# Kernel optimization log

Measured on AMD Instinct MI355X. Metric: run time of the kernel, lower is better.

Reference implementation:

```python
import jax, jax.numpy as jnp
import numpy as np

V = 256  # vec_size
B = 128  # batch
T = 1024  # seq_len


def _lstm_layer(x_seq, W_ih, W_hh, b_ih, b_hh):
    # x_seq: [B, T, V]; weights follow torch LSTMCell layout: W_* [4V, V], gate order i,f,g,o
    x_proj = jnp.einsum('btv,gv->btg', x_seq, W_ih) + b_ih + b_hh  # [B, T, 4V]
    x_proj = jnp.transpose(x_proj, (1, 0, 2))  # time-major [T, B, 4V]
    Bsz = x_seq.shape[0]
    Vd = W_hh.shape[1]
    h0 = jnp.zeros((Bsz, Vd), x_seq.dtype)
    c0 = jnp.zeros((Bsz, Vd), x_seq.dtype)

    def step(carry, xp):
        h, c = carry
        gates = xp + h @ W_hh.T  # [B, 4V]
        i, f, g, o = jnp.split(gates, 4, axis=-1)
        i = jax.nn.sigmoid(i)
        f = jax.nn.sigmoid(f)
        g = jnp.tanh(g)
        o = jax.nn.sigmoid(o)
        c = f * c + i * g
        h = o * jnp.tanh(c)
        return (h, c), h

    _, hs = jax.lax.scan(step, (h0, c0), x_proj)  # hs: [T, B, V]
    return jnp.transpose(hs, (1, 0, 2))  # [B, T, V]


def setup_inputs() -> dict:
    key = jax.random.key(0)
    ks = jax.random.split(key, 12)
    s = 1.0 / np.sqrt(V)  # torch LSTMCell / Linear init scale
    u = lambda k, shape: jax.random.uniform(k, shape, jnp.float32, -s, s)
    return {
        'x': jax.random.normal(ks[0], (B, T, V), jnp.float32),
        'W_ih1': u(ks[1], (4 * V, V)), 'W_hh1': u(ks[2], (4 * V, V)),
        'b_ih1': u(ks[3], (4 * V,)), 'b_hh1': u(ks[4], (4 * V,)),
        'W_ih2': u(ks[5], (4 * V, V)), 'W_hh2': u(ks[6], (4 * V, V)),
        'b_ih2': u(ks[7], (4 * V,)), 'b_hh2': u(ks[8], (4 * V,)),
        'fc_w': u(ks[9], (V, V)), 'fc_b': u(ks[10], (V,)),
    }


def reference(x, W_ih1, W_hh1, b_ih1, b_hh1, W_ih2, W_hh2, b_ih2, b_hh2, fc_w, fc_b):
    h1s = _lstm_layer(x, W_ih1, W_hh1, b_ih1, b_hh1)      # [B, T, V]
    h2s = _lstm_layer(h1s, W_ih2, W_hh2, b_ih2, b_hh2)    # [B, T, V]
    # NormalizedLinear: linear with L2 row-normalized weight
    w_n = fc_w / jnp.linalg.norm(fc_w, axis=1, keepdims=True)
    out = jnp.einsum('btv,ov->bto', h2s, w_n) + fc_b
    return out
```

## Files before the change

kernel.cpp:

```cpp
#include <hip/hip_runtime.h>
#include <stdint.h>

#define Tt 1024
#define Bt 128
#define Vt 256
#define TS 32768

typedef __attribute__((ext_vector_type(8))) short bf16x8;
typedef __attribute__((ext_vector_type(4))) float f32x4;
typedef __attribute__((ext_vector_type(4))) int i32x4;

#define MFMA(a, b, c) __builtin_amdgcn_mfma_f32_16x16x32_bf16(a, b, c, 0, 0, 0)
#define SENT 0x7FFF


__device__ __forceinline__ unsigned short f2bf(float f) {
    unsigned u = __builtin_bit_cast(unsigned, f);
    u += 0x7fffu + ((u >> 16) & 1u);
    return (unsigned short)(u >> 16);
}
__device__ __forceinline__ float sigm(float x) {
    return __builtin_amdgcn_rcpf(1.f + __expf(-x));
}
__device__ __forceinline__ float tanh_f(float x) {
    float e = __expf(-2.f * fabsf(x));
    float t = (1.f - e) * __builtin_amdgcn_rcpf(1.f + e);
    return copysignf(t, x);
}

template <int OFF>
__device__ __forceinline__ bf16x8 ldcc(const unsigned short* p) {
    bf16x8 d;
    asm volatile("global_load_dwordx4 %0, %1, off offset:%c2 sc0 sc1"
                 : "=v"(d) : "v"(p), "i"(OFF));
    return d;
}
#define LD8T(d, P)                                        \
    do {                                                  \
        const unsigned short* _p2 = (P) + 2048;           \
        d[0] = ldcc<0>(P);      d[1] = ldcc<1024>(P);     \
        d[2] = ldcc<2048>(P);   d[3] = ldcc<3072>(P);     \
        d[4] = ldcc<0>(_p2);    d[5] = ldcc<1024>(_p2);   \
        d[6] = ldcc<2048>(_p2); d[7] = ldcc<3072>(_p2);   \
    } while (0)

__device__ __forceinline__ void vm_drain() {
    asm volatile("s_waitcnt vmcnt(0)" ::: "memory");
    __builtin_amdgcn_sched_barrier(0);
}
__device__ __forceinline__ int fdirty(bf16x8 f) {
    i32x4 d = __builtin_bit_cast(i32x4, f);
    return ((d.x & 0xFFFF) == SENT) | ((d.z & 0xFFFF) == SENT);
}

__global__ __launch_bounds__(256) void cvt_kernel(const float* __restrict__ x,
                                                  unsigned short* __restrict__ xT) {
    unsigned g = blockIdx.x * 256u + threadIdx.x;
    unsigned base = g * 8u;
    unsigned r = base >> 8;
    unsigned v = base & 255u;
    unsigned t = r >> 7, b = r & 127u;
    const float4* src = (const float4*)(x + ((size_t)b * Tt + t) * Vt + v);
    float4 f0 = src[0], f1 = src[1];
    union { unsigned short s[8]; int4 q; } o;
    o.s[0] = f2bf(f0.x); o.s[1] = f2bf(f0.y); o.s[2] = f2bf(f0.z); o.s[3] = f2bf(f0.w);
    o.s[4] = f2bf(f1.x); o.s[5] = f2bf(f1.y); o.s[6] = f2bf(f1.z); o.s[7] = f2bf(f1.w);
    *(int4*)(xT + (size_t)r * Vt + v) = o.q;
}

__global__ __launch_bounds__(256) void fill_kernel(unsigned short* __restrict__ h) {
    size_t i = ((size_t)blockIdx.x * 256u + threadIdx.x) * 16u;
    i32x4 s = (i32x4){0x7FFF7FFF, 0x7FFF7FFF, 0x7FFF7FFF, 0x7FFF7FFF};
    *(i32x4*)(h + i) = s;
    *(i32x4*)(h + i + 8) = s;
}

__global__ __launch_bounds__(256) void rec_kernel(
    const float* __restrict__ Wih1, const float* __restrict__ Whh1,
    const float* __restrict__ bih1, const float* __restrict__ bhh1,
    const float* __restrict__ Wih2, const float* __restrict__ Whh2,
    const float* __restrict__ bih2, const float* __restrict__ bhh2,
    const unsigned short* __restrict__ xT,
    unsigned short* h1s, unsigned short* h2s) {
    const int bid = blockIdx.x;
    const int layer = bid >> 6;
    const int cgrp = (bid >> 3) & 7;
    const int bgrp = bid & 7;

    const float* Win = layer ? Wih2 : Wih1;
    const float* Whh = layer ? Whh2 : Whh1;
    const float* bi = layer ? bih2 : bih1;
    const float* bh = layer ? bhh2 : bhh1;

    __shared__ unsigned short sW[2][128][264];
    __shared__ float sG[4][16][36];
    __shared__ unsigned short sH[16][32];

    const int tid = threadIdx.x;
    {
        int row = tid >> 1, seg = (tid & 1) * 128;
        size_t grow = (size_t)(256 * (row >> 5) + 32 * cgrp + (row & 31)) * Vt + seg;
        for (int m = 0; m < 2; ++m) {
            const float* src = (m ? Whh : Win) + grow;
            unsigned short* dst = &sW[m][row][seg];
            for (int k = 0; k < 128; k += 4) {
                float4 f = *(const float4*)(src + k);
                dst[k + 0] = f2bf(f.x); dst[k + 1] = f2bf(f.y);
                dst[k + 2] = f2bf(f.z); dst[k + 3] = f2bf(f.w);
            }
        }
    }
    __syncthreads();

    const int lane = tid & 63;
    const int wv = tid >> 6;
    const int q = lane >> 4;
    const int ln = lane & 15;

    float biasv[2];
#pragma unroll
    for (int n = 0; n < 2; ++n) {
        int grow = 256 * wv + 32 * cgrp + n * 16 + ln;
        biasv[n] = bi[grow] + bh[grow];
    }
    const int cb = tid >> 4;
    const int cc0 = (tid & 15) * 2;
    float cst[2] = {0.f, 0.f};

    const int aoff = ln * 32 + q * 8;
    const size_t hbase = (size_t)bgrp * 4096 + aoff;
    const int xoff = (16 * bgrp + ln) * 256 + q * 8;
    unsigned short* ob = layer ? h2s : h1s;
    unsigned short* sptr = ob + (size_t)bgrp * 4096 + cgrp * 512 + lane * 8;

    for (int t = 0; t < Tt; ++t) {
        f32x4 acc[2];
        acc[0] = (f32x4){biasv[0], biasv[0], biasv[0], biasv[0]};
        acc[1] = (f32x4){biasv[1], biasv[1], biasv[1], biasv[1]};
        bf16x8 a1[8], a2[8];

        if (layer == 0) {
            const unsigned short* xp = xT + (size_t)t * TS + xoff;
#pragma unroll
            for (int kb = 0; kb < 8; ++kb) a1[kb] = *(const bf16x8*)(xp + kb * 32);
            const unsigned short* hp = h1s + (size_t)(t - 1) * TS + hbase;
            if (t > 0) LD8T(a2, hp);
#pragma unroll
            for (int kb = 0; kb < 8; ++kb) {
                bf16x8 b0 = *(const bf16x8*)&sW[0][32 * wv + ln][kb * 32 + q * 8];
                bf16x8 b1 = *(const bf16x8*)&sW[0][32 * wv + 16 + ln][kb * 32 + q * 8];
                acc[0] = MFMA(a1[kb], b0, acc[0]);
                acc[1] = MFMA(a1[kb], b1, acc[1]);
            }
            if (t > 0) {
                for (;;) {
                    vm_drain();
                    int d = 0;
#pragma unroll
                    for (int kb = 0; kb < 8; ++kb) d |= fdirty(a2[kb]);
                    if (!__any(d)) break;
                    __builtin_amdgcn_s_sleep(1);
                    LD8T(a2, hp);
                }
#pragma unroll
                for (int kb = 0; kb < 8; ++kb) {
                    bf16x8 b0 = *(const bf16x8*)&sW[1][32 * wv + ln][kb * 32 + q * 8];
                    bf16x8 b1 = *(const bf16x8*)&sW[1][32 * wv + 16 + ln][kb * 32 + q * 8];
                    acc[0] = MFMA(a2[kb], b0, acc[0]);
                    acc[1] = MFMA(a2[kb], b1, acc[1]);
                }
            }
        } else {
            const unsigned short* hp1 = h1s + (size_t)t * TS + hbase;
            const unsigned short* hp2 = h2s + (size_t)(t - 1) * TS + hbase;
            LD8T(a1, hp1);
            if (t > 0) LD8T(a2, hp2);
            unsigned need = (t > 0) ? 3u : 1u;
            for (;;) {
                vm_drain();
                unsigned nm = 0;
                if (need & 1) {
                    int d = 0;
#pragma unroll
                    for (int kb = 0; kb < 8; ++kb) d |= fdirty(a1[kb]);
                    if (__any(d)) nm |= 1u;
                }
                if (need & 2) {
                    int d = 0;
#pragma unroll
                    for (int kb = 0; kb < 8; ++kb) d |= fdirty(a2[kb]);
                    if (__any(d)) nm |= 2u;
                }
                if (!nm) break;
                need = nm;
                __builtin_amdgcn_s_sleep(1);
                if (nm & 1) LD8T(a1, hp1);
                if (nm & 2) LD8T(a2, hp2);
            }
#pragma unroll
            for (int kb = 0; kb < 8; ++kb) {
                bf16x8 b0 = *(const bf16x8*)&sW[0][32 * wv + ln][kb * 32 + q * 8];
                bf16x8 b1 = *(const bf16x8*)&sW[0][32 * wv + 16 + ln][kb * 32 + q * 8];
                acc[0] = MFMA(a1[kb], b0, acc[0]);
                acc[1] = MFMA(a1[kb], b1, acc[1]);
            }
            if (t > 0) {
#pragma unroll
                for (int kb = 0; kb < 8; ++kb) {
                    bf16x8 b0 = *(const bf16x8*)&sW[1][32 * wv + ln][kb * 32 + q * 8];
                    bf16x8 b1 = *(const bf16x8*)&sW[1][32 * wv + 16 + ln][kb * 32 + q * 8];
                    acc[0] = MFMA(a2[kb], b0, acc[0]);
                    acc[1] = MFMA(a2[kb], b1, acc[1]);
                }
            }
        }

#pragma unroll
        for (int n = 0; n < 2; ++n)
#pragma unroll
            for (int r = 0; r < 4; ++r) sG[wv][q * 4 + r][n * 16 + ln] = acc[n][r];
        __syncthreads();
#pragma unroll
        for (int j = 0; j < 2; ++j) {
            int c = cc0 + j;
            float iv = sG[0][cb][c], fv = sG[1][cb][c];
            float gv = sG[2][cb][c], ov = sG[3][cb][c];
            float cval = sigm(fv) * cst[j] + sigm(iv) * tanh_f(gv);
            cst[j] = cval;
            sH[cb][c] = f2bf(sigm(ov) * tanh_f(cval));
        }
        __syncthreads();
        if (tid < 64) {
            bf16x8 hv = *(const bf16x8*)((const unsigned short*)sH + tid * 8);
            unsigned short* dst = sptr + (size_t)t * TS;
            asm volatile("global_store_dwordx4 %0, %1, off sc0 sc1" ::"v"(dst),
                         "v"(hv) : "memory");
        }
    }
}

__global__ __launch_bounds__(256) void fc_kernel(const unsigned short* __restrict__ h2s,
                                                 const float* __restrict__ fcw,
                                                 const float* __restrict__ fcb,
                                                 float* __restrict__ out) {
    const int bid = blockIdx.x;
    const int rb = bid >> 2;
    const int c0 = (bid & 3) * 64;
    __shared__ unsigned short sWf[64][264];
    __shared__ float sInv[64];
    const int tid = threadIdx.x;
    if (tid < 64) {
        const float* wr = fcw + (size_t)(c0 + tid) * 256;
        float s = 0.f;
        for (int k = 0; k < 256; k += 4) {
            float4 f = *(const float4*)(wr + k);
            s += f.x * f.x + f.y * f.y + f.z * f.z + f.w * f.w;
        }
        sInv[tid] = rsqrtf(s);
    }
    __syncthreads();
    {
        int lr = tid & 63, seg = tid >> 6;
        float inv = sInv[lr];
        const float* wr = fcw + (size_t)(c0 + lr) * 256 + seg * 64;
        unsigned short* dst = &sWf[lr][seg * 64];
        for (int k = 0; k < 64; k += 4) {
            float4 f = *(const float4*)(wr + k);
            dst[k + 0] = f2bf(f.x * inv); dst[k + 1] = f2bf(f.y * inv);
            dst[k + 2] = f2bf(f.z * inv); dst[k + 3] = f2bf(f.w * inv);
        }
    }
    __syncthreads();
    const int lane = tid & 63, w = tid >> 6, q = lane >> 4, ln = lane & 15;
    f32x4 acc[2][4];
    for (int rk = 0; rk < 2; ++rk)
        for (int nb = 0; nb < 4; ++nb) {
            float bv = fcb[c0 + nb * 16 + ln];
            acc[rk][nb] = (f32x4){bv, bv, bv, bv};
        }
    const unsigned short* P0 =
        h2s + (size_t)rb * TS + (2 * w) * 4096 + ln * 32 + q * 8;
    const unsigned short* P1 = P0 + 4096;
    for (int kb = 0; kb < 8; ++kb) {
        bf16x8 a0 = *(const bf16x8*)(P0 + kb * 512);
        bf16x8 a1 = *(const bf16x8*)(P1 + kb * 512);
        for (int nb = 0; nb < 4; ++nb) {
            bf16x8 b = *(const bf16x8*)&sWf[nb * 16 + ln][kb * 32 + q * 8];
            acc[0][nb] = MFMA(a0, b, acc[0][nb]);
            acc[1][nb] = MFMA(a1, b, acc[1][nb]);
        }
    }
    for (int rk = 0; rk < 2; ++rk)
        for (int nb = 0; nb < 4; ++nb)
            for (int r = 0; r < 4; ++r) {
                int bb = 32 * w + rk * 16 + q * 4 + r;
                int o = c0 + nb * 16 + ln;
                out[((size_t)bb * Tt + rb) * 256 + o] = acc[rk][nb][r];
            }
}

extern "C" void kernel_launch(void* const* d_in, const int* in_sizes, int n_in,
                              void* d_out, int out_size, void* d_ws, size_t ws_size,
                              hipStream_t stream) {
    const float* x    = (const float*)d_in[0];
    const float* Wih1 = (const float*)d_in[1];
    const float* Whh1 = (const float*)d_in[2];
    const float* bih1 = (const float*)d_in[3];
    const float* bhh1 = (const float*)d_in[4];
    const float* Wih2 = (const float*)d_in[5];
    const float* Whh2 = (const float*)d_in[6];
    const float* bih2 = (const float*)d_in[7];
    const float* bhh2 = (const float*)d_in[8];
    const float* fcw  = (const float*)d_in[9];
    const float* fcb  = (const float*)d_in[10];

    char* ws = (char*)d_ws;
    unsigned short* xT  = (unsigned short*)ws;
    unsigned short* h1s = xT + (size_t)Tt * TS;
    unsigned short* h2s = h1s + (size_t)Tt * TS;

    fill_kernel<<<16384, 256, 0, stream>>>(h1s);
    cvt_kernel<<<16384, 256, 0, stream>>>(x, xT);
    rec_kernel<<<128, 256, 0, stream>>>(Wih1, Whh1, bih1, bhh1,
                                        Wih2, Whh2, bih2, bhh2,
                                        xT, h1s, h2s);
    fc_kernel<<<4096, 256, 0, stream>>>(h2s, fcw, fcb, (float*)d_out);
}
```

Baseline: 3.107 ms.

## Reorder gate rows per wave so LSTM cell update stays in-wave without block barriers

Weight rows in shared memory are regrouped so each wave holds all four gates (i,f,g,o) for its own 8 hidden columns. The cell update then happens in registers via a lane shuffle instead of through a shared-memory gate exchange. This removes both per-timestep __syncthreads from the recurrent loop, and each wave stores its own h slice. The hidden-state memory layout changes to match, and the FC kernel's addressing is updated to the same layout.

```diff
diff --git a/kernel.cpp b/kernel.cpp
--- a/kernel.cpp
+++ b/kernel.cpp
@@ -92,17 +92,17 @@
     const float* bi = layer ? bih2 : bih1;
     const float* bh = layer ? bhh2 : bhh1;
 
-    __shared__ unsigned short sW[2][128][264];
-    __shared__ float sG[4][16][36];
-    __shared__ unsigned short sH[16][32];
+    __shared__ unsigned short sW[2][4][32][264];
+    __shared__ unsigned short sH[4][16][8];
 
     const int tid = threadIdx.x;
     {
         int row = tid >> 1, seg = (tid & 1) * 128;
-        size_t grow = (size_t)(256 * (row >> 5) + 32 * cgrp + (row & 31)) * Vt + seg;
+        int wvs = row >> 5, lr = row & 31, gate = lr >> 3, loc = lr & 7;
+        size_t grow = (size_t)(256 * gate + 32 * cgrp + 8 * wvs + loc) * Vt + seg;
         for (int m = 0; m < 2; ++m) {
             const float* src = (m ? Whh : Win) + grow;
-            unsigned short* dst = &sW[m][row][seg];
+            unsigned short* dst = &sW[m][wvs][lr][seg];
             for (int k = 0; k < 128; k += 4) {
                 float4 f = *(const float4*)(src + k);
                 dst[k + 0] = f2bf(f.x); dst[k + 1] = f2bf(f.y);
@@ -119,19 +119,18 @@
 
     float biasv[2];
 #pragma unroll
-    for (int n = 0; n < 2; ++n) {
-        int grow = 256 * wv + 32 * cgrp + n * 16 + ln;
-        biasv[n] = bi[grow] + bh[grow];
-    }
-    const int cb = tid >> 4;
-    const int cc0 = (tid & 15) * 2;
-    float cst[2] = {0.f, 0.f};
-
-    const int aoff = ln * 32 + q * 8;
-    const size_t hbase = (size_t)bgrp * 4096 + aoff;
+    for (int nb = 0; nb < 2; ++nb) {
+        int gate = nb * 2 + (ln >> 3);
+        int grow = 256 * gate + 32 * cgrp + 8 * wv + (ln & 7);
+        biasv[nb] = bi[grow] + bh[grow];
+    }
+    float cst[4] = {0.f, 0.f, 0.f, 0.f};
+
+    const size_t hbase = (size_t)bgrp * 4096 + q * 128 + ln * 8;
     const int xoff = (16 * bgrp + ln) * 256 + q * 8;
     unsigned short* ob = layer ? h2s : h1s;
-    unsigned short* sptr = ob + (size_t)bgrp * 4096 + cgrp * 512 + lane * 8;
+    unsigned short* sptr =
+        ob + (size_t)bgrp * 4096 + cgrp * 512 + wv * 128 + lane * 8;
 
     for (int t = 0; t < Tt; ++t) {
         f32x4 acc[2];
@@ -147,8 +146,8 @@
             if (t > 0) LD8T(a2, hp);
 #pragma unroll
             for (int kb = 0; kb < 8; ++kb) {
-                bf16x8 b0 = *(const bf16x8*)&sW[0][32 * wv + ln][kb * 32 + q * 8];
-                bf16x8 b1 = *(const bf16x8*)&sW[0][32 * wv + 16 + ln][kb * 32 + q * 8];
+                bf16x8 b0 = *(const bf16x8*)&sW[0][wv][ln][kb * 32 + q * 8];
+                bf16x8 b1 = *(const bf16x8*)&sW[0][wv][16 + ln][kb * 32 + q * 8];
                 acc[0] = MFMA(a1[kb], b0, acc[0]);
                 acc[1] = MFMA(a1[kb], b1, acc[1]);
             }
@@ -164,8 +163,8 @@
                 }
 #pragma unroll
                 for (int kb = 0; kb < 8; ++kb) {
-                    bf16x8 b0 = *(const bf16x8*)&sW[1][32 * wv + ln][kb * 32 + q * 8];
-                    bf16x8 b1 = *(const bf16x8*)&sW[1][32 * wv + 16 + ln][kb * 32 + q * 8];
+                    bf16x8 b0 = *(const bf16x8*)&sW[1][wv][ln][kb * 32 + q * 8];
+                    bf16x8 b1 = *(const bf16x8*)&sW[1][wv][16 + ln][kb * 32 + q * 8];
                     acc[0] = MFMA(a2[kb], b0, acc[0]);
                     acc[1] = MFMA(a2[kb], b1, acc[1]);
                 }
@@ -199,16 +198,16 @@
             }
 #pragma unroll
             for (int kb = 0; kb < 8; ++kb) {
-                bf16x8 b0 = *(const bf16x8*)&sW[0][32 * wv + ln][kb * 32 + q * 8];
-                bf16x8 b1 = *(const bf16x8*)&sW[0][32 * wv + 16 + ln][kb * 32 + q * 8];
+                bf16x8 b0 = *(const bf16x8*)&sW[0][wv][ln][kb * 32 + q * 8];
+                bf16x8 b1 = *(const bf16x8*)&sW[0][wv][16 + ln][kb * 32 + q * 8];
                 acc[0] = MFMA(a1[kb], b0, acc[0]);
                 acc[1] = MFMA(a1[kb], b1, acc[1]);
             }
             if (t > 0) {
 #pragma unroll
                 for (int kb = 0; kb < 8; ++kb) {
-                    bf16x8 b0 = *(const bf16x8*)&sW[1][32 * wv + ln][kb * 32 + q * 8];
-                    bf16x8 b1 = *(const bf16x8*)&sW[1][32 * wv + 16 + ln][kb * 32 + q * 8];
+                    bf16x8 b0 = *(const bf16x8*)&sW[1][wv][ln][kb * 32 + q * 8];
+                    bf16x8 b1 = *(const bf16x8*)&sW[1][wv][16 + ln][kb * 32 + q * 8];
                     acc[0] = MFMA(a2[kb], b0, acc[0]);
                     acc[1] = MFMA(a2[kb], b1, acc[1]);
                 }
@@ -216,22 +215,22 @@
         }
 
 #pragma unroll
-        for (int n = 0; n < 2; ++n)
-#pragma unroll
-            for (int r = 0; r < 4; ++r) sG[wv][q * 4 + r][n * 16 + ln] = acc[n][r];
-        __syncthreads();
-#pragma unroll
-        for (int j = 0; j < 2; ++j) {
-            int c = cc0 + j;
-            float iv = sG[0][cb][c], fv = sG[1][cb][c];
-            float gv = sG[2][cb][c], ov = sG[3][cb][c];
-            float cval = sigm(fv) * cst[j] + sigm(iv) * tanh_f(gv);
-            cst[j] = cval;
-            sH[cb][c] = f2bf(sigm(ov) * tanh_f(cval));
-        }
-        __syncthreads();
-        if (tid < 64) {
-            bf16x8 hv = *(const bf16x8*)((const unsigned short*)sH + tid * 8);
+        for (int r = 0; r < 4; ++r) {
+            float a0 = acc[0][r], a1v = acc[1][r];
+            float b0 = __shfl_xor(a0, 8), b1 = __shfl_xor(a1v, 8);
+            float iv, fv, gv, ov;
+            if (ln < 8) { iv = a0; fv = b0; gv = a1v; ov = b1; }
+            else        { iv = b0; fv = a0; gv = b1; ov = a1v; }
+            float ii = sigm(iv), ff = sigm(fv), gg = tanh_f(gv), oo = sigm(ov);
+            float cc = ff * cst[r] + ii * gg;
+            cst[r] = cc;
+            float hh = oo * tanh_f(cc);
+            if (ln < 8) sH[wv][q * 4 + r][ln] = f2bf(hh);
+        }
+        asm volatile("s_waitcnt lgkmcnt(0)" ::: "memory");
+        __builtin_amdgcn_sched_barrier(0);
+        if (lane < 16) {
+            bf16x8 hv = *(const bf16x8*)&sH[wv][lane][0];
             unsigned short* dst = sptr + (size_t)t * TS;
             asm volatile("global_store_dwordx4 %0, %1, off sc0 sc1" ::"v"(dst),
                          "v"(hv) : "memory");
@@ -278,8 +277,7 @@
             float bv = fcb[c0 + nb * 16 + ln];
             acc[rk][nb] = (f32x4){bv, bv, bv, bv};
         }
-    const unsigned short* P0 =
-        h2s + (size_t)rb * TS + (2 * w) * 4096 + ln * 32 + q * 8;
+    const unsigned short* P0 = h2s + (size_t)rb * TS + (2 * w) * 4096 + q * 128 + ln * 8;
     const unsigned short* P1 = P0 + 4096;
     for (int kb = 0; kb < 8; ++kb) {
         bf16x8 a0 = *(const bf16x8*)(P0 + kb * 512);
```

After: 3.351 ms. 7.9% more time.

## Split recurrent matmul over K across wave pairs, fuse gate math in registers

Applied to the files above, without the earlier changes.

Work per block is now split so each wave covers all four gates for 16 columns and half of the K dimension, not one gate over the full K. Partial sums from the upper-K waves go through shared memory and are added into the lower-K waves, which then compute the LSTM cell update directly from their accumulators. This removes the full gate-scatter through shared memory and halves the global h/x loads each wave waits on per step, shortening the serial critical path. The cost is extra partial-sum traffic, half the waves sitting idle during the elementwise phase, and a different wave issuing the store.

```diff
diff --git a/kernel.cpp b/kernel.cpp
--- a/kernel.cpp
+++ b/kernel.cpp
@@ -35,13 +35,10 @@
                  : "=v"(d) : "v"(p), "i"(OFF));
     return d;
 }
-#define LD8T(d, P)                                        \
-    do {                                                  \
-        const unsigned short* _p2 = (P) + 2048;           \
-        d[0] = ldcc<0>(P);      d[1] = ldcc<1024>(P);     \
-        d[2] = ldcc<2048>(P);   d[3] = ldcc<3072>(P);     \
-        d[4] = ldcc<0>(_p2);    d[5] = ldcc<1024>(_p2);   \
-        d[6] = ldcc<2048>(_p2); d[7] = ldcc<3072>(_p2);   \
+#define LD4T(d, P)                                      \
+    do {                                                \
+        d[0] = ldcc<0>(P);    d[1] = ldcc<1024>(P);     \
+        d[2] = ldcc<2048>(P); d[3] = ldcc<3072>(P);     \
     } while (0)
 
 __device__ __forceinline__ void vm_drain() {
@@ -93,7 +90,7 @@
     const float* bh = layer ? bhh2 : bhh1;
 
     __shared__ unsigned short sW[2][128][264];
-    __shared__ float sG[4][16][36];
+    __shared__ float sP[2][4][16][20];
     __shared__ unsigned short sH[16][32];
 
     const int tid = threadIdx.x;
@@ -114,67 +111,69 @@
 
     const int lane = tid & 63;
     const int wv = tid >> 6;
+    const int cs = wv >> 1;
+    const int ks = wv & 1;
     const int q = lane >> 4;
     const int ln = lane & 15;
 
-    float biasv[2];
-#pragma unroll
-    for (int n = 0; n < 2; ++n) {
-        int grow = 256 * wv + 32 * cgrp + n * 16 + ln;
-        biasv[n] = bi[grow] + bh[grow];
-    }
-    const int cb = tid >> 4;
-    const int cc0 = (tid & 15) * 2;
-    float cst[2] = {0.f, 0.f};
-
-    const int aoff = ln * 32 + q * 8;
-    const size_t hbase = (size_t)bgrp * 4096 + aoff;
-    const int xoff = (16 * bgrp + ln) * 256 + q * 8;
+    float biasv[4];
+#pragma unroll
+    for (int nb = 0; nb < 4; ++nb) {
+        int grow = 256 * nb + 32 * cgrp + 16 * cs + ln;
+        biasv[nb] = ks ? 0.f : (bi[grow] + bh[grow]);
+    }
+    float cst[4] = {0.f, 0.f, 0.f, 0.f};
+
+    const size_t hbase = (size_t)bgrp * 4096 + ks * 2048 + ln * 32 + q * 8;
+    const int xoff = (16 * bgrp + ln) * 256 + 128 * ks + q * 8;
     unsigned short* ob = layer ? h2s : h1s;
     unsigned short* sptr = ob + (size_t)bgrp * 4096 + cgrp * 512 + lane * 8;
 
     for (int t = 0; t < Tt; ++t) {
-        f32x4 acc[2];
-        acc[0] = (f32x4){biasv[0], biasv[0], biasv[0], biasv[0]};
-        acc[1] = (f32x4){biasv[1], biasv[1], biasv[1], biasv[1]};
-        bf16x8 a1[8], a2[8];
+        f32x4 acc[4];
+#pragma unroll
+        for (int nb = 0; nb < 4; ++nb)
+            acc[nb] = (f32x4){biasv[nb], biasv[nb], biasv[nb], biasv[nb]};
+        bf16x8 a1[4], a2[4];
 
         if (layer == 0) {
             const unsigned short* xp = xT + (size_t)t * TS + xoff;
 #pragma unroll
-            for (int kb = 0; kb < 8; ++kb) a1[kb] = *(const bf16x8*)(xp + kb * 32);
+            for (int j = 0; j < 4; ++j) a1[j] = *(const bf16x8*)(xp + j * 32);
             const unsigned short* hp = h1s + (size_t)(t - 1) * TS + hbase;
-            if (t > 0) LD8T(a2, hp);
-#pragma unroll
-            for (int kb = 0; kb < 8; ++kb) {
-                bf16x8 b0 = *(const bf16x8*)&sW[0][32 * wv + ln][kb * 32 + q * 8];
-                bf16x8 b1 = *(const bf16x8*)&sW[0][32 * wv + 16 + ln][kb * 32 + q * 8];
-                acc[0] = MFMA(a1[kb], b0, acc[0]);
-                acc[1] = MFMA(a1[kb], b1, acc[1]);
-            }
+            if (t > 0) LD4T(a2, hp);
+#pragma unroll
+            for (int kbl = 0; kbl < 4; ++kbl)
+#pragma unroll
+                for (int nb = 0; nb < 4; ++nb) {
+                    bf16x8 b = *(const bf16x8*)
+                        &sW[0][nb * 32 + 16 * cs + ln][128 * ks + kbl * 32 + q * 8];
+                    acc[nb] = MFMA(a1[kbl], b, acc[nb]);
+                }
             if (t > 0) {
                 for (;;) {
                     vm_drain();
                     int d = 0;
 #pragma unroll
-                    for (int kb = 0; kb < 8; ++kb) d |= fdirty(a2[kb]);
+                    for (int j = 0; j < 4; ++j) d |= fdirty(a2[j]);
                     if (!__any(d)) break;
                     __builtin_amdgcn_s_sleep(1);
-                    LD8T(a2, hp);
-                }
-#pragma unroll
-                for (int kb = 0; kb < 8; ++kb) {
-                    bf16x8 b0 = *(const bf16x8*)&sW[1][32 * wv + ln][kb * 32 + q * 8];
-                    bf16x8 b1 = *(const bf16x8*)&sW[1][32 * wv + 16 + ln][kb * 32 + q * 8];
-                    acc[0] = MFMA(a2[kb], b0, acc[0]);
-                    acc[1] = MFMA(a2[kb], b1, acc[1]);
-                }
+                    LD4T(a2, hp);
+                }
+#pragma unroll
+                for (int kbl = 0; kbl < 4; ++kbl)
+#pragma unroll
+                    for (int nb = 0; nb < 4; ++nb) {
+                        bf16x8 b = *(const bf16x8*)
+                            &sW[1][nb * 32 + 16 * cs + ln][128 * ks + kbl * 32 + q * 8];
+                        acc[nb] = MFMA(a2[kbl], b, acc[nb]);
+                    }
             }
         } else {
             const unsigned short* hp1 = h1s + (size_t)t * TS + hbase;
             const unsigned short* hp2 = h2s + (size_t)(t - 1) * TS + hbase;
-            LD8T(a1, hp1);
-            if (t > 0) LD8T(a2, hp2);
+            LD4T(a1, hp1);
+            if (t > 0) LD4T(a2, hp2);
             unsigned need = (t > 0) ? 3u : 1u;
             for (;;) {
                 vm_drain();
@@ -182,56 +181,63 @@
                 if (need & 1) {
                     int d = 0;
 #pragma unroll
-                    for (int kb = 0; kb < 8; ++kb) d |= fdirty(a1[kb]);
+                    for (int j = 0; j < 4; ++j) d |= fdirty(a1[j]);
                     if (__any(d)) nm |= 1u;
                 }
                 if (need & 2) {
                     int d = 0;
 #pragma unroll
-                    for (int kb = 0; kb < 8; ++kb) d |= fdirty(a2[kb]);
+                    for (int j = 0; j < 4; ++j) d |= fdirty(a2[j]);
                     if (__any(d)) nm |= 2u;
                 }
                 if (!nm) break;
                 need = nm;
                 __builtin_amdgcn_s_sleep(1);
-                if (nm & 1) LD8T(a1, hp1);
-                if (nm & 2) LD8T(a2, hp2);
-            }
-#pragma unroll
-            for (int kb = 0; kb < 8; ++kb) {
-                bf16x8 b0 = *(const bf16x8*)&sW[0][32 * wv + ln][kb * 32 + q * 8];
-                bf16x8 b1 = *(const bf16x8*)&sW[0][32 * wv + 16 + ln][kb * 32 + q * 8];
-                acc[0] = MFMA(a1[kb], b0, acc[0]);
-                acc[1] = MFMA(a1[kb], b1, acc[1]);
-            }
+                if (nm & 1) LD4T(a1, hp1);
+                if (nm & 2) LD4T(a2, hp2);
+            }
+#pragma unroll
+            for (int kbl = 0; kbl < 4; ++kbl)
+#pragma unroll
+                for (int nb = 0; nb < 4; ++nb) {
+                    bf16x8 b = *(const bf16x8*)
+                        &sW[0][nb * 32 + 16 * cs + ln][128 * ks + kbl * 32 + q * 8];
+                    acc[nb] = MFMA(a1[kbl], b, acc[nb]);
+                }
             if (t > 0) {
 #pragma unroll
-                for (int kb = 0; kb < 8; ++kb) {
-                    bf16x8 b0 = *(const bf16x8*)&sW[1][32 * wv + ln][kb * 32 + q * 8];
-                    bf16x8 b1 = *(const bf16x8*)&sW[1][32 * wv + 16 + ln][kb * 32 + q * 8];
-                    acc[0] = MFMA(a2[kb], b0, acc[0]);
-                    acc[1] = MFMA(a2[kb], b1, acc[1]);
-                }
-            }
-        }
-
-#pragma unroll
-        for (int n = 0; n < 2; ++n)
-#pragma unroll
-            for (int r = 0; r < 4; ++r) sG[wv][q * 4 + r][n * 16 + ln] = acc[n][r];
+                for (int kbl = 0; kbl < 4; ++kbl)
+#pragma unroll
+                    for (int nb = 0; nb < 4; ++nb) {
+                        bf16x8 b = *(const bf16x8*)
+                            &sW[1][nb * 32 + 16 * cs + ln][128 * ks + kbl * 32 + q * 8];
+                        acc[nb] = MFMA(a2[kbl], b, acc[nb]);
+                    }
+            }
+        }
+
+        if (ks) {
+#pragma unroll
+            for (int nb = 0; nb < 4; ++nb)
+                *(f32x4*)&sP[cs][nb][ln][q * 4] = acc[nb];
+        }
         __syncthreads();
-#pragma unroll
-        for (int j = 0; j < 2; ++j) {
-            int c = cc0 + j;
-            float iv = sG[0][cb][c], fv = sG[1][cb][c];
-            float gv = sG[2][cb][c], ov = sG[3][cb][c];
-            float cval = sigm(fv) * cst[j] + sigm(iv) * tanh_f(gv);
-            cst[j] = cval;
-            sH[cb][c] = f2bf(sigm(ov) * tanh_f(cval));
+        if (!ks) {
+#pragma unroll
+            for (int nb = 0; nb < 4; ++nb)
+                acc[nb] += *(const f32x4*)&sP[cs][nb][ln][q * 4];
+#pragma unroll
+            for (int r = 0; r < 4; ++r) {
+                float iv = acc[0][r], fv = acc[1][r];
+                float gv = acc[2][r], ov = acc[3][r];
+                float cc = sigm(fv) * cst[r] + sigm(iv) * tanh_f(gv);
+                cst[r] = cc;
+                sH[q * 4 + r][16 * cs + ln] = f2bf(sigm(ov) * tanh_f(cc));
+            }
         }
         __syncthreads();
-        if (tid < 64) {
-            bf16x8 hv = *(const bf16x8*)((const unsigned short*)sH + tid * 8);
+        if (wv == 1) {
+            bf16x8 hv = *(const bf16x8*)((const unsigned short*)sH + lane * 8);
             unsigned short* dst = sptr + (size_t)t * TS;
             asm volatile("global_store_dwordx4 %0, %1, off sc0 sc1" ::"v"(dst),
                          "v"(hv) : "memory");
```

Result: faster. 2.866 ms (-7.8%).
